# Kernel optimization log

Measured on AMD Instinct MI355X. Metric: run time of the kernel, lower is better.

## Reference

```python
import jax, jax.numpy as jnp
import numpy as np

DIM = 128
BATCH = 1048576
EPS = 1e-08


def setup_inputs() -> dict:
    key = jax.random.key(0)
    k1, k2 = jax.random.split(key)
    x = jax.random.normal(k1, (BATCH, DIM), dtype=jnp.float32)
    v_vectors = jax.random.normal(k2, (DIM, DIM), dtype=jnp.float32)
    scale = jnp.ones((1,), dtype=jnp.float32)
    diag_scale = jnp.ones((DIM,), dtype=jnp.float32)
    return {"x": x, "v_vectors": v_vectors, "scale": scale, "diag_scale": diag_scale}


def _build_Q(v_vectors, eps=EPS):
    # Q = H(v_0) @ H(v_1) @ ... @ H(v_{dim-1}), v_i = columns of v_vectors.
    # Q @ (I - 2 v v^T) = Q - 2 (Q v) v^T  -> avoid forming each H explicitly,
    # identical math to the original loop.
    dim = v_vectors.shape[0]
    vs = v_vectors.T  # rows of vs == columns of v_vectors, scan order preserved

    def step(Q, v):
        v = v / (jnp.linalg.norm(v) + eps)
        Qv = Q @ v
        return Q - 2.0 * jnp.outer(Qv, v), None

    Q0 = jnp.eye(dim, dtype=v_vectors.dtype)
    Q, _ = jax.lax.scan(step, Q0, vs)
    return Q


def reference(x, v_vectors, scale, diag_scale):
    Q = _build_Q(v_vectors)
    s = scale[0]
    # W = (Q @ diag(diag_scale)) * s  == Q scaled column-wise
    W = Q * (diag_scale * s)
    y = x @ W  # [B, dim]
    logdet = jnp.sum(jnp.log(jnp.abs(diag_scale * s) + EPS))
    return y, logdet
```

## Files before the change

### kernel.cpp

```cpp
#include <hip/hip_runtime.h>
#include <math.h>

#define DIM 128
#define BATCH 1048576
#define WT_STRIDE 136

typedef float f32x4 __attribute__((ext_vector_type(4)));
typedef short bf16x8 __attribute__((ext_vector_type(8)));

__device__ __forceinline__ unsigned short f2bf(float f) {
    unsigned u = __builtin_bit_cast(unsigned, f);
    u += 0x7FFFu + ((u >> 16) & 1u);
    return (unsigned short)(u >> 16);
}

__global__ __launch_bounds__(256) void build_w_kernel(
    const float* __restrict__ vvec,
    const float* __restrict__ scale_p,
    const float* __restrict__ diag,
    unsigned short* __restrict__ wt,
    float* __restrict__ logdet_out)
{
    __shared__ float vt[DIM * 129];
    __shared__ float part[2 * DIM];
    __shared__ float scale_sh;

    const int t    = threadIdx.x;
    const int r    = t & 127;
    const int half = t >> 7;
    const int c0   = half * 64;

    for (int idx = t; idx < DIM * DIM; idx += 256) {
        int j = idx >> 7;
        int i = idx & 127;
        vt[i * 129 + j] = vvec[idx];
    }

    float q[64];
    #pragma unroll
    for (int j = 0; j < 64; ++j) q[j] = (c0 + j == r) ? 1.0f : 0.0f;

    __syncthreads();

    for (int i = 0; i < DIM; ++i) {
        const float* v = &vt[i * 129];

        if (t < 64) {
            float a = v[t], b = v[t + 64];
            float ss = a * a + b * b;
            #pragma unroll
            for (int m = 32; m >= 1; m >>= 1) ss += __shfl_xor(ss, m, 64);
            if (t == 0) scale_sh = 1.0f / (sqrtf(ss) + 1e-8f);
        }

        float dot = 0.0f;
        #pragma unroll
        for (int j = 0; j < 64; ++j) dot += q[j] * v[c0 + j];
        part[half * DIM + r] = dot;
        __syncthreads();

        const float sc   = scale_sh;
        const float coef = 2.0f * sc * sc * (part[r] + part[DIM + r]);
        #pragma unroll
        for (int j = 0; j < 64; ++j) q[j] -= coef * v[c0 + j];
        __syncthreads();
    }

    const float s = scale_p[0];
    #pragma unroll
    for (int j = 0; j < 64; ++j) {
        const int c = c0 + j;
        wt[c * WT_STRIDE + r] = f2bf(q[j] * diag[c] * s);
    }

    if (t == 0) {
        float ld = 0.0f;
        for (int c = 0; c < DIM; ++c) ld += logf(fabsf(diag[c] * s) + 1e-8f);
        *logdet_out = ld;
    }
}

__global__ __launch_bounds__(256) void gemm_kernel(
    const float* __restrict__ x,
    const unsigned short* __restrict__ wt,
    float* __restrict__ y)
{
    __shared__ unsigned short wlds[DIM * WT_STRIDE];

    const int t = threadIdx.x;

    const int total4 = DIM * WT_STRIDE / 8;
    for (int idx = t; idx < total4; idx += 256) {
        ((f32x4*)wlds)[idx] = ((const f32x4*)wt)[idx];
    }
    __syncthreads();

    const int wave = t >> 6;
    const int lane = t & 63;
    const int n15  = lane & 15;
    const int quad = lane >> 4;

    const long rowbase = (long)blockIdx.x * 128 + wave * 32;

    f32x4 xa[2][8];
    #pragma unroll
    for (int rt = 0; rt < 2; ++rt) {
        const float* xrow = x + (rowbase + rt * 16 + n15) * DIM + quad * 8;
        #pragma unroll
        for (int kc = 0; kc < 4; ++kc) {
            xa[rt][kc * 2]     = *(const f32x4*)(xrow + kc * 32);
            xa[rt][kc * 2 + 1] = *(const f32x4*)(xrow + kc * 32 + 4);
        }
    }

    f32x4 acc[2][8];
    #pragma unroll
    for (int rt = 0; rt < 2; ++rt)
        #pragma unroll
        for (int ct = 0; ct < 8; ++ct)
            acc[rt][ct] = (f32x4)0.0f;

    #pragma unroll
    for (int kc = 0; kc < 4; ++kc) {
        bf16x8 afrag[2];
        #pragma unroll
        for (int rt = 0; rt < 2; ++rt) {
            const f32x4 lo = xa[rt][kc * 2];
            const f32x4 hi = xa[rt][kc * 2 + 1];
            bf16x8 f;
            f[0] = (short)f2bf(lo[0]); f[1] = (short)f2bf(lo[1]);
            f[2] = (short)f2bf(lo[2]); f[3] = (short)f2bf(lo[3]);
            f[4] = (short)f2bf(hi[0]); f[5] = (short)f2bf(hi[1]);
            f[6] = (short)f2bf(hi[2]); f[7] = (short)f2bf(hi[3]);
            afrag[rt] = f;
        }
        const int koff = kc * 32 + quad * 8;
        #pragma unroll
        for (int ct = 0; ct < 8; ++ct) {
            const bf16x8 bfrag = *(const bf16x8*)&wlds[(ct * 16 + n15) * WT_STRIDE + koff];
            acc[0][ct] = __builtin_amdgcn_mfma_f32_16x16x32_bf16(afrag[0], bfrag, acc[0][ct], 0, 0, 0);
            acc[1][ct] = __builtin_amdgcn_mfma_f32_16x16x32_bf16(afrag[1], bfrag, acc[1][ct], 0, 0, 0);
        }
    }

    #pragma unroll
    for (int rt = 0; rt < 2; ++rt) {
        #pragma unroll
        for (int reg = 0; reg < 4; ++reg) {
            float* yrow = y + (rowbase + rt * 16 + quad * 4 + reg) * DIM;
            #pragma unroll
            for (int ct = 0; ct < 8; ++ct) {
                yrow[ct * 16 + n15] = acc[rt][ct][reg];
            }
        }
    }
}

extern "C" void kernel_launch(void* const* d_in, const int* in_sizes, int n_in,
                              void* d_out, int out_size, void* d_ws, size_t ws_size,
                              hipStream_t stream) {
    const float* x     = (const float*)d_in[0];
    const float* vvec  = (const float*)d_in[1];
    const float* scale = (const float*)d_in[2];
    const float* diag  = (const float*)d_in[3];

    float* y = (float*)d_out;
    float* logdet = y + (size_t)BATCH * DIM;
    unsigned short* wt = (unsigned short*)d_ws;

    build_w_kernel<<<1, 256, 0, stream>>>(vvec, scale, diag, wt, logdet);
    gemm_kernel<<<BATCH / 128, 256, 0, stream>>>(x, wt, y);
}
```

Before: 1.013 ms.

## Persistent GEMM with double-buffered x loads and barrier-free Householder build

The GEMM becomes a persistent kernel with a fixed grid of 512 blocks. Each block loads W into LDS once and walks many row tiles, prefetching the next tile of x into registers while the current tile is computed and stored. The single-block W build is remapped so each pair of adjacent lanes owns one row of Q. Every thread now computes the vector norm redundantly and the two half-dots are combined with a shuffle, which removes the shared-memory partials and both barriers per Householder step. The cost is higher register pressure from the two x buffers, the new launch-bounds hints, and less latency hiding across blocks with a small grid.

```diff
diff --git a/kernel.cpp b/kernel.cpp
--- a/kernel.cpp
+++ b/kernel.cpp
@@ -4,6 +4,10 @@
 #define DIM 128
 #define BATCH 1048576
 #define WT_STRIDE 136
+#define VT_STRIDE 132
+#define GEMM_GRID 512
+#define NTILES (BATCH / 128)
+#define TILES_PER_BLOCK (NTILES / GEMM_GRID)
 
 typedef float f32x4 __attribute__((ext_vector_type(4)));
 typedef short bf16x8 __attribute__((ext_vector_type(8)));
@@ -14,26 +18,24 @@
     return (unsigned short)(u >> 16);
 }
 
-__global__ __launch_bounds__(256) void build_w_kernel(
+__global__ __launch_bounds__(256, 1) void build_w_kernel(
     const float* __restrict__ vvec,
     const float* __restrict__ scale_p,
     const float* __restrict__ diag,
     unsigned short* __restrict__ wt,
     float* __restrict__ logdet_out)
 {
-    __shared__ float vt[DIM * 129];
-    __shared__ float part[2 * DIM];
-    __shared__ float scale_sh;
+    __shared__ float vt[DIM * VT_STRIDE];
 
     const int t    = threadIdx.x;
-    const int r    = t & 127;
-    const int half = t >> 7;
-    const int c0   = half * 64;
+    const int r    = t >> 1;
+    const int c0   = (t & 1) * 64;
+    const int lane = t & 63;
 
     for (int idx = t; idx < DIM * DIM; idx += 256) {
         int j = idx >> 7;
         int i = idx & 127;
-        vt[i * 129 + j] = vvec[idx];
+        vt[i * VT_STRIDE + j] = vvec[idx];
     }
 
     float q[64];
@@ -43,27 +45,36 @@
     __syncthreads();
 
     for (int i = 0; i < DIM; ++i) {
-        const float* v = &vt[i * 129];
-
-        if (t < 64) {
-            float a = v[t], b = v[t + 64];
-            float ss = a * a + b * b;
-            #pragma unroll
-            for (int m = 32; m >= 1; m >>= 1) ss += __shfl_xor(ss, m, 64);
-            if (t == 0) scale_sh = 1.0f / (sqrtf(ss) + 1e-8f);
-        }
-
-        float dot = 0.0f;
-        #pragma unroll
-        for (int j = 0; j < 64; ++j) dot += q[j] * v[c0 + j];
-        part[half * DIM + r] = dot;
-        __syncthreads();
-
-        const float sc   = scale_sh;
-        const float coef = 2.0f * sc * sc * (part[r] + part[DIM + r]);
-        #pragma unroll
-        for (int j = 0; j < 64; ++j) q[j] -= coef * v[c0 + j];
-        __syncthreads();
+        const float* __restrict__ v = &vt[i * VT_STRIDE];
+
+        float na = v[lane], nb = v[lane + 64];
+        float ss = na * na + nb * nb;
+        #pragma unroll
+        for (int m = 32; m >= 1; m >>= 1) ss += __shfl_xor(ss, m, 64);
+        const float sc = 1.0f / (sqrtf(ss) + 1e-8f);
+
+        float vv[64];
+        #pragma unroll
+        for (int k = 0; k < 16; ++k) {
+            f32x4 w = *(const f32x4*)(v + c0 + 4 * k);
+            vv[4*k]   = w[0]; vv[4*k+1] = w[1];
+            vv[4*k+2] = w[2]; vv[4*k+3] = w[3];
+        }
+
+        float d0 = 0.f, d1 = 0.f, d2 = 0.f, d3 = 0.f;
+        #pragma unroll
+        for (int k = 0; k < 16; ++k) {
+            d0 += q[4*k]   * vv[4*k];
+            d1 += q[4*k+1] * vv[4*k+1];
+            d2 += q[4*k+2] * vv[4*k+2];
+            d3 += q[4*k+3] * vv[4*k+3];
+        }
+        float dot = (d0 + d1) + (d2 + d3);
+        dot += __shfl_xor(dot, 1, 64);
+
+        const float coef = 2.0f * sc * sc * dot;
+        #pragma unroll
+        for (int j = 0; j < 64; ++j) q[j] -= coef * vv[j];
     }
 
     const float s = scale_p[0];
@@ -73,14 +84,16 @@
         wt[c * WT_STRIDE + r] = f2bf(q[j] * diag[c] * s);
     }
 
-    if (t == 0) {
-        float ld = 0.0f;
-        for (int c = 0; c < DIM; ++c) ld += logf(fabsf(diag[c] * s) + 1e-8f);
-        *logdet_out = ld;
-    }
-}
-
-__global__ __launch_bounds__(256) void gemm_kernel(
+    if (t < 64) {
+        float ld = logf(fabsf(diag[t] * s) + 1e-8f)
+                 + logf(fabsf(diag[t + 64] * s) + 1e-8f);
+        #pragma unroll
+        for (int m = 32; m >= 1; m >>= 1) ld += __shfl_xor(ld, m, 64);
+        if (t == 0) *logdet_out = ld;
+    }
+}
+
+__global__ __launch_bounds__(256, 2) void gemm_kernel(
     const float* __restrict__ x,
     const unsigned short* __restrict__ wt,
     float* __restrict__ y)
@@ -93,66 +106,84 @@
     for (int idx = t; idx < total4; idx += 256) {
         ((f32x4*)wlds)[idx] = ((const f32x4*)wt)[idx];
     }
-    __syncthreads();
 
     const int wave = t >> 6;
     const int lane = t & 63;
     const int n15  = lane & 15;
     const int quad = lane >> 4;
 
-    const long rowbase = (long)blockIdx.x * 128 + wave * 32;
-
-    f32x4 xa[2][8];
-    #pragma unroll
-    for (int rt = 0; rt < 2; ++rt) {
-        const float* xrow = x + (rowbase + rt * 16 + n15) * DIM + quad * 8;
+    auto loadx = [&](f32x4 (&xb)[2][8], int tileIdx) {
+        const long rowbase = (long)tileIdx * 128 + wave * 32;
+        #pragma unroll
+        for (int rt = 0; rt < 2; ++rt) {
+            const float* xrow = x + (rowbase + rt * 16 + n15) * DIM + quad * 8;
+            #pragma unroll
+            for (int kc = 0; kc < 4; ++kc) {
+                xb[rt][kc * 2]     = *(const f32x4*)(xrow + kc * 32);
+                xb[rt][kc * 2 + 1] = *(const f32x4*)(xrow + kc * 32 + 4);
+            }
+        }
+    };
+
+    auto compute_store = [&](const f32x4 (&xb)[2][8], int tileIdx) {
+        const long rowbase = (long)tileIdx * 128 + wave * 32;
+
+        f32x4 acc[2][8];
+        #pragma unroll
+        for (int rt = 0; rt < 2; ++rt)
+            #pragma unroll
+            for (int ct = 0; ct < 8; ++ct)
+                acc[rt][ct] = (f32x4)0.0f;
+
         #pragma unroll
         for (int kc = 0; kc < 4; ++kc) {
-            xa[rt][kc * 2]     = *(const f32x4*)(xrow + kc * 32);
-            xa[rt][kc * 2 + 1] = *(const f32x4*)(xrow + kc * 32 + 4);
-        }
-    }
-
-    f32x4 acc[2][8];
-    #pragma unroll
-    for (int rt = 0; rt < 2; ++rt)
-        #pragma unroll
-        for (int ct = 0; ct < 8; ++ct)
-            acc[rt][ct] = (f32x4)0.0f;
-
-    #pragma unroll
-    for (int kc = 0; kc < 4; ++kc) {
-        bf16x8 afrag[2];
+            bf16x8 afrag[2];
+            #pragma unroll
+            for (int rt = 0; rt < 2; ++rt) {
+                const f32x4 lo = xb[rt][kc * 2];
+                const f32x4 hi = xb[rt][kc * 2 + 1];
+                bf16x8 f;
+                f[0] = (short)f2bf(lo[0]); f[1] = (short)f2bf(lo[1]);
+                f[2] = (short)f2bf(lo[2]); f[3] = (short)f2bf(lo[3]);
+                f[4] = (short)f2bf(hi[0]); f[5] = (short)f2bf(hi[1]);
+                f[6] = (short)f2bf(hi[2]); f[7] = (short)f2bf(hi[3]);
+                afrag[rt] = f;
+            }
+            const int koff = kc * 32 + quad * 8;
+            #pragma unroll
+            for (int ct = 0; ct < 8; ++ct) {
+                const bf16x8 bfrag = *(const bf16x8*)&wlds[(ct * 16 + n15) * WT_STRIDE + koff];
+                acc[0][ct] = __builtin_amdgcn_mfma_f32_16x16x32_bf16(afrag[0], bfrag, acc[0][ct], 0, 0, 0);
+                acc[1][ct] = __builtin_amdgcn_mfma_f32_16x16x32_bf16(afrag[1], bfrag, acc[1][ct], 0, 0, 0);
+            }
+        }
+
         #pragma unroll
         for (int rt = 0; rt < 2; ++rt) {
-            const f32x4 lo = xa[rt][kc * 2];
-            const f32x4 hi = xa[rt][kc * 2 + 1];
-            bf16x8 f;
-            f[0] = (short)f2bf(lo[0]); f[1] = (short)f2bf(lo[1]);
-            f[2] = (short)f2bf(lo[2]); f[3] = (short)f2bf(lo[3]);
-            f[4] = (short)f2bf(hi[0]); f[5] = (short)f2bf(hi[1]);
-            f[6] = (short)f2bf(hi[2]); f[7] = (short)f2bf(hi[3]);
-            afrag[rt] = f;
-        }
-        const int koff = kc * 32 + quad * 8;
-        #pragma unroll
-        for (int ct = 0; ct < 8; ++ct) {
-            const bf16x8 bfrag = *(const bf16x8*)&wlds[(ct * 16 + n15) * WT_STRIDE + koff];
-            acc[0][ct] = __builtin_amdgcn_mfma_f32_16x16x32_bf16(afrag[0], bfrag, acc[0][ct], 0, 0, 0);
-            acc[1][ct] = __builtin_amdgcn_mfma_f32_16x16x32_bf16(afrag[1], bfrag, acc[1][ct], 0, 0, 0);
-        }
-    }
-
-    #pragma unroll
-    for (int rt = 0; rt < 2; ++rt) {
-        #pragma unroll
-        for (int reg = 0; reg < 4; ++reg) {
-            float* yrow = y + (rowbase + rt * 16 + quad * 4 + reg) * DIM;
-            #pragma unroll
-            for (int ct = 0; ct < 8; ++ct) {
-                yrow[ct * 16 + n15] = acc[rt][ct][reg];
-            }
-        }
+            #pragma unroll
+            for (int reg = 0; reg < 4; ++reg) {
+                float* yrow = y + (rowbase + rt * 16 + quad * 4 + reg) * DIM;
+                #pragma unroll
+                for (int ct = 0; ct < 8; ++ct) {
+                    yrow[ct * 16 + n15] = acc[rt][ct][reg];
+                }
+            }
+        }
+    };
+
+    f32x4 xa[2][8], xb[2][8];
+
+    loadx(xa, blockIdx.x);
+    __syncthreads();
+
+    for (int kk = 0; kk < TILES_PER_BLOCK / 2; ++kk) {
+        const int t0 = blockIdx.x + (2 * kk)     * GEMM_GRID;
+        const int t1 = blockIdx.x + (2 * kk + 1) * GEMM_GRID;
+        loadx(xb, t1);
+        compute_store(xa, t0);
+        if (kk + 1 < TILES_PER_BLOCK / 2)
+            loadx(xa, blockIdx.x + (2 * kk + 2) * GEMM_GRID);
+        compute_store(xb, t1);
     }
 }
 
@@ -169,5 +200,5 @@
     unsigned short* wt = (unsigned short*)d_ws;
 
     build_w_kernel<<<1, 256, 0, stream>>>(vvec, scale, diag, wt, logdet);
-    gemm_kernel<<<BATCH / 128, 256, 0, stream>>>(x, wt, y);
-}
+    gemm_kernel<<<GEMM_GRID, 256, 0, stream>>>(x, wt, y);
+}
```

Result: faster. 964.4 us (-4.8%).
